# Kernel optimization log

Measured on AMD Instinct MI355X. Metric: run time of the kernel, lower is better.

The kernel has to match this reference:

```python
import jax, jax.numpy as jnp
import numpy as np

B, S, D, H, E, K, F = 8, 2048, 1024, 16, 32, 8, 1024
HD = D // H
EPS = 1e-5


def _ln(x, scale, bias):
    m = jnp.mean(x, axis=-1, keepdims=True)
    v = jnp.mean(jnp.square(x - m), axis=-1, keepdims=True)
    return (x - m) * jax.lax.rsqrt(v + EPS) * scale + bias


def setup_inputs() -> dict:
    key = jax.random.key(0)
    ks = jax.random.split(key, 14)
    w = lambda k, shp: jax.random.normal(k, shp, jnp.float32) * 0.02
    return {
        "hidden_states": jax.random.normal(ks[0], (B, S, D), jnp.float32),
        "ln1_scale": jnp.ones((D,), jnp.float32),
        "ln1_bias": jnp.zeros((D,), jnp.float32),
        "wq": w(ks[1], (D, D)), "bq": jnp.zeros((D,), jnp.float32),
        "wk": w(ks[2], (D, D)), "bk": jnp.zeros((D,), jnp.float32),
        "wv": w(ks[3], (D, D)), "bv": jnp.zeros((D,), jnp.float32),
        "ln2_scale": jnp.ones((D,), jnp.float32),
        "ln2_bias": jnp.zeros((D,), jnp.float32),
        "router_w": w(ks[4], (D, E)), "router_b": jnp.zeros((E,), jnp.float32),
        "w1": w(ks[5], (E, D, F)), "b1": jnp.zeros((E, F), jnp.float32),
        "w2": w(ks[6], (E, F, D)), "b2": jnp.zeros((E, D), jnp.float32),
    }


def reference(hidden_states, ln1_scale, ln1_bias, wq, bq, wk, bk, wv, bv,
              ln2_scale, ln2_bias, router_w, router_b, w1, b1, w2, b2):
    # --- attention sub-block (faithful to source: scores are [B,S,H,H]) ---
    x = _ln(hidden_states, ln1_scale, ln1_bias)
    q = (x @ wq + bq).reshape(B, S, H, HD)
    k = (x @ wk + bk).reshape(B, S, H, HD)
    v = (x @ wv + bv).reshape(B, S, H, HD)
    scores = jnp.einsum('bshd,bsgd->bshg', q, k) / np.sqrt(HD).astype(np.float32)
    probs = jax.nn.softmax(scores, axis=-1)
    ctx = jnp.einsum('bshg,bsgd->bshd', probs, v).reshape(B, S, D)
    h1 = hidden_states + ctx
    # --- MoE sub-block: per-token top-K of E experts ---
    x2 = _ln(h1, ln2_scale, ln2_bias)
    router_probs = jax.nn.softmax(x2 @ router_w + router_b, axis=-1)  # [B,S,E]
    top_w, top_i = jax.lax.top_k(router_probs, K)
    top_w = top_w / jnp.sum(top_w, axis=-1, keepdims=True)
    # dense per-token gate over experts (zero for unselected)
    gates = jnp.sum(jax.nn.one_hot(top_i, E, dtype=x2.dtype) * top_w[..., None], axis=-2)  # [B,S,E]
    moe = jnp.zeros_like(x2)
    for e in range(E):  # fixed small expert set; unrolled under jit
        h = jax.nn.gelu(x2 @ w1[e] + b1[e], approximate=False)
        moe = moe + gates[..., e:e + 1] * (h @ w2[e] + b2[e])
    return h1 + moe
```

## Files before the change

kernel.cpp:

```cpp
#include <hip/hip_runtime.h>
#include <hip/hip_bf16.h>
#include <stdint.h>

#define TOK 16384
#define DD  1024
#define NE  32

typedef unsigned short u16;
typedef __attribute__((ext_vector_type(8))) short short8;
typedef __attribute__((ext_vector_type(8))) unsigned short u16x8;
typedef __attribute__((ext_vector_type(4))) float f32x4;

__device__ __forceinline__ u16 f2bf(float f) {
  unsigned int u = __float_as_uint(f);
  u += 0x7fffu + ((u >> 16) & 1u);
  return (u16)(u >> 16);
}
__device__ __forceinline__ float bf2f(u16 h) {
  return __uint_as_float(((unsigned int)h) << 16);
}
__device__ __forceinline__ void gload16(const void* g, void* l) {
  __builtin_amdgcn_global_load_lds((const __attribute__((address_space(1))) void*)g,
                                   (__attribute__((address_space(3))) void*)l, 16, 0, 0);
}
__device__ __forceinline__ float fast_gelu(float v) {
  float s = v * 0.70710678118f;
  float a = fabsf(s);
  float t = 1.0f / fmaf(0.3275911f, a, 1.0f);
  float poly = t * fmaf(t, fmaf(t, fmaf(t, fmaf(t, 1.061405429f, -1.453152027f),
                                        1.421413741f), -0.284496736f), 0.254829592f);
  float er = 1.0f - poly * __expf(-s * s);
  er = copysignf(er, s);
  return 0.5f * v * (1.0f + er);
}

__global__ __launch_bounds__(256) void k_transpose(const float* __restrict__ src,
                                                   u16* __restrict__ dst, int R, int C) {
  __shared__ float tile[32][33];
  size_t mb = (size_t)blockIdx.z * R * C;
  int c0 = blockIdx.x * 32, r0 = blockIdx.y * 32;
  int tx = threadIdx.x, ty = threadIdx.y;
#pragma unroll
  for (int i = 0; i < 4; i++)
    tile[ty + i * 8][tx] = src[mb + (size_t)(r0 + ty + i * 8) * C + c0 + tx];
  __syncthreads();
#pragma unroll
  for (int i = 0; i < 4; i++) {
    float v = tile[tx][ty + i * 8];
    dst[mb + (size_t)(c0 + ty + i * 8) * R + r0 + tx] = f2bf(v);
  }
}

__global__ __launch_bounds__(256) void k_transpose_split(const float* __restrict__ src,
                                                         u16* __restrict__ hi,
                                                         u16* __restrict__ lo, int R, int C) {
  __shared__ float tile[32][33];
  int c0 = blockIdx.x * 32, r0 = blockIdx.y * 32;
  int tx = threadIdx.x, ty = threadIdx.y;
#pragma unroll
  for (int i = 0; i < 4; i++)
    tile[ty + i * 8][tx] = src[(size_t)(r0 + ty + i * 8) * C + c0 + tx];
  __syncthreads();
#pragma unroll
  for (int i = 0; i < 4; i++) {
    float v = tile[tx][ty + i * 8];
    u16 h = f2bf(v);
    u16 l = f2bf(v - bf2f(h));
    size_t idx = (size_t)(c0 + ty + i * 8) * R + r0 + tx;
    hi[idx] = h;
    lo[idx] = l;
  }
}

__global__ __launch_bounds__(256) void k_ln1(const float* __restrict__ x,
                                             const float* __restrict__ sc,
                                             const float* __restrict__ bi,
                                             u16* __restrict__ ohi, u16* __restrict__ olo) {
  __shared__ float red[10];
  int t = blockIdx.x, tid = threadIdx.x;
  size_t base = (size_t)t * DD + tid * 4;
  float4 v = *(const float4*)(x + base);
  float s1 = v.x + v.y + v.z + v.w;
  float s2 = v.x * v.x + v.y * v.y + v.z * v.z + v.w * v.w;
  for (int o = 1; o < 64; o <<= 1) { s1 += __shfl_xor(s1, o, 64); s2 += __shfl_xor(s2, o, 64); }
  int wid = tid >> 6;
  if ((tid & 63) == 0) { red[wid * 2] = s1; red[wid * 2 + 1] = s2; }
  __syncthreads();
  if (tid == 0) {
    float a = 0, b = 0;
    for (int i = 0; i < 4; i++) { a += red[i * 2]; b += red[i * 2 + 1]; }
    float mean = a * (1.f / DD);
    float var = b * (1.f / DD) - mean * mean;
    red[8] = mean; red[9] = rsqrtf(var + 1e-5f);
  }
  __syncthreads();
  float mean = red[8], rs = red[9];
  int e0 = tid * 4;
  float xv[4] = {v.x, v.y, v.z, v.w};
  ushort4 oh, ol;
  u16* ph = (u16*)&oh; u16* pl = (u16*)&ol;
#pragma unroll
  for (int i = 0; i < 4; i++) {
    float f = (xv[i] - mean) * rs * sc[e0 + i] + bi[e0 + i];
    u16 h = f2bf(f);
    ph[i] = h;
    pl[i] = f2bf(f - bf2f(h));
  }
  *(ushort4*)(ohi + base) = oh;
  *(ushort4*)(olo + base) = ol;
}

__global__ __launch_bounds__(256) void k_attn(
    const float* __restrict__ hidden, const float* __restrict__ qb,
    const float* __restrict__ kb, const float* __restrict__ vb,
    const float* __restrict__ ln2s, const float* __restrict__ ln2b,
    float* __restrict__ out, u16* __restrict__ x2hi, u16* __restrict__ x2lo) {
  __shared__ float qs[16][68], ks[16][68], vs[16][68];
  __shared__ float probs[16][17];
  __shared__ float red[12];
  int t = blockIdx.x, tid = threadIdx.x;
  size_t base = (size_t)t * DD + tid * 4;
  int hh = tid >> 4, dd = (tid & 15) * 4;
  {
    float4 q4 = *(const float4*)(qb + base);
    float4 k4 = *(const float4*)(kb + base);
    float4 v4 = *(const float4*)(vb + base);
    qs[hh][dd + 0] = q4.x; qs[hh][dd + 1] = q4.y; qs[hh][dd + 2] = q4.z; qs[hh][dd + 3] = q4.w;
    ks[hh][dd + 0] = k4.x; ks[hh][dd + 1] = k4.y; ks[hh][dd + 2] = k4.z; ks[hh][dd + 3] = k4.w;
    vs[hh][dd + 0] = v4.x; vs[hh][dd + 1] = v4.y; vs[hh][dd + 2] = v4.z; vs[hh][dd + 3] = v4.w;
  }
  __syncthreads();
  {
    int g = tid & 15;
    float s = 0.f;
#pragma unroll
    for (int d = 0; d < 64; d++) s += qs[hh][d] * ks[g][d];
    s *= 0.125f;
    float mx = s;
    for (int o = 1; o < 16; o <<= 1) mx = fmaxf(mx, __shfl_xor(mx, o, 16));
    float p = __expf(s - mx);
    float sm = p;
    for (int o = 1; o < 16; o <<= 1) sm += __shfl_xor(sm, o, 16);
    probs[hh][g] = p / sm;
  }
  __syncthreads();
  float c0 = 0, c1 = 0, c2 = 0, c3 = 0;
#pragma unroll
  for (int g = 0; g < 16; g++) {
    float pw = probs[hh][g];
    c0 += pw * vs[g][dd + 0]; c1 += pw * vs[g][dd + 1];
    c2 += pw * vs[g][dd + 2]; c3 += pw * vs[g][dd + 3];
  }
  float4 hv = *(const float4*)(hidden + base);
  float h0 = hv.x + c0, h1 = hv.y + c1, h2 = hv.z + c2, h3 = hv.w + c3;
  { float4 o4; o4.x = h0; o4.y = h1; o4.z = h2; o4.w = h3; *(float4*)(out + base) = o4; }
  float s1 = h0 + h1 + h2 + h3;
  float s2 = h0 * h0 + h1 * h1 + h2 * h2 + h3 * h3;
  for (int o = 1; o < 64; o <<= 1) { s1 += __shfl_xor(s1, o, 64); s2 += __shfl_xor(s2, o, 64); }
  int wid = tid >> 6;
  if ((tid & 63) == 0) { red[wid * 2] = s1; red[wid * 2 + 1] = s2; }
  __syncthreads();
  if (tid == 0) {
    float a = 0, b = 0;
    for (int i = 0; i < 4; i++) { a += red[i * 2]; b += red[i * 2 + 1]; }
    float mean = a * (1.f / DD);
    float var = b * (1.f / DD) - mean * mean;
    red[8] = mean; red[9] = rsqrtf(var + 1e-5f);
  }
  __syncthreads();
  float mean = red[8], rs = red[9];
  int e0 = tid * 4;
  float hvv[4] = {h0, h1, h2, h3};
  ushort4 oh, ol;
  u16* ph = (u16*)&oh; u16* pl = (u16*)&ol;
#pragma unroll
  for (int i = 0; i < 4; i++) {
    float f = (hvv[i] - mean) * rs * ln2s[e0 + i] + ln2b[e0 + i];
    u16 h = f2bf(f);
    ph[i] = h;
    pl[i] = f2bf(f - bf2f(h));
  }
  *(ushort4*)(x2hi + base) = oh;
  *(ushort4*)(x2lo + base) = ol;
}

__global__ __launch_bounds__(256) void k_router(
    const u16* __restrict__ Xhi, const u16* __restrict__ Xlo,
    const u16* __restrict__ Bh_, const u16* __restrict__ Bl_,
    const float* __restrict__ rb, float* __restrict__ logits) {
  __shared__ alignas(16) u16 Ah[64 * 32], Al[64 * 32], Bh[32 * 32], Bl[32 * 32];
  int tid = threadIdx.x;
  int w = tid >> 6, lane = tid & 63;
  int t0 = (int)blockIdx.x * 64;
  int row = tid >> 2, q = tid & 3;
  int cb = tid & 127, rowb = cb >> 2, qb2 = cb & 3;
  f32x4 acc[2];
  acc[0] = (f32x4)0.f; acc[1] = (f32x4)0.f;
  const int la = lane & 15, lk = (lane >> 4) * 8;
  const int m0 = w * 16;
  for (int kt = 0; kt < 32; kt++) {
    int k0 = kt * 32;
    __syncthreads();
    gload16(Xhi + (size_t)(t0 + row) * DD + k0 + q * 8, (char*)Ah + tid * 16);
    gload16(Xlo + (size_t)(t0 + row) * DD + k0 + q * 8, (char*)Al + tid * 16);
    if (tid < 128)
      gload16(Bh_ + (size_t)rowb * DD + k0 + qb2 * 8, (char*)Bh + cb * 16);
    else
      gload16(Bl_ + (size_t)rowb * DD + k0 + qb2 * 8, (char*)Bl + cb * 16);
    __syncthreads();
    short8 ah = *(const short8*)&Ah[(m0 + la) * 32 + lk];
    short8 al = *(const short8*)&Al[(m0 + la) * 32 + lk];
#pragma unroll
    for (int n = 0; n < 2; n++) {
      short8 bh = *(const short8*)&Bh[(n * 16 + la) * 32 + lk];
      short8 bl = *(const short8*)&Bl[(n * 16 + la) * 32 + lk];
      acc[n] = __builtin_amdgcn_mfma_f32_16x16x32_bf16(ah, bh, acc[n], 0, 0, 0);
      acc[n] = __builtin_amdgcn_mfma_f32_16x16x32_bf16(ah, bl, acc[n], 0, 0, 0);
      acc[n] = __builtin_amdgcn_mfma_f32_16x16x32_bf16(al, bh, acc[n], 0, 0, 0);
    }
  }
  int rl4 = (lane >> 4) * 4;
#pragma unroll
  for (int n = 0; n < 2; n++) {
    int col = n * 16 + la;
    float bias = rb[col];
#pragma unroll
    for (int r = 0; r < 4; r++) {
      int grow = t0 + m0 + rl4 + r;
      logits[(size_t)grow * NE + col] = acc[n][r] + bias;
    }
  }
}

__global__ void k_zero32(int* p) { int i = threadIdx.x; if (i < 32) p[i] = 0; }

__global__ __launch_bounds__(256) void k_topk(
    const float* __restrict__ logits, int* __restrict__ counts,
    int* __restrict__ lists, int* __restrict__ slots, float* __restrict__ gsel) {
  int tid = threadIdx.x;
  int t = blockIdx.x * 8 + (tid >> 5);
  int e = tid & 31;
  int sub = (tid >> 5) & 1;
  float l = logits[(size_t)t * NE + e];
  float mx = l;
  for (int o = 1; o < 32; o <<= 1) mx = fmaxf(mx, __shfl_xor(mx, o, 32));
  float p = __expf(l - mx);
  float sm = p;
  for (int o = 1; o < 32; o <<= 1) sm += __shfl_xor(sm, o, 32);
  p /= sm;
  bool sel = false;
#pragma unroll
  for (int r = 0; r < 8; r++) {
    float bv = sel ? -1.f : p;
    int bi_ = e;
    for (int o = 1; o < 32; o <<= 1) {
      float ov = __shfl_xor(bv, o, 32);
      int oi = __shfl_xor(bi_, o, 32);
      if (ov > bv || (ov == bv && oi < bi_)) { bv = ov; bi_ = oi; }
    }
    if (e == bi_) sel = true;
  }
  float ts = sel ? p : 0.f;
  for (int o = 1; o < 32; o <<= 1) ts += __shfl_xor(ts, o, 32);
  unsigned long long bm = __ballot(sel);
  unsigned m32 = (unsigned)(bm >> (sub * 32));
  if (sel) {
    int j = __popc(m32 & ((1u << e) - 1u));
    int pos = atomicAdd(&counts[e], 1);
    lists[(size_t)e * TOK + pos] = t;
    slots[t * 8 + j] = (e << 14) | pos;
    gsel[t * 8 + j] = p / ts;
  }
}

__global__ void k_scan(const int* __restrict__ counts, int* __restrict__ segoff) {
  if (threadIdx.x == 0) { int s = 0; for (int e = 0; e < NE; e++) { segoff[e] = s; s += counts[e]; } }
}

__global__ __launch_bounds__(256) void k_gemm_p(
    const u16* __restrict__ Ahi, const u16* __restrict__ Alo,
    const u16* __restrict__ qkvT,
    const float* __restrict__ bq, const float* __restrict__ bk, const float* __restrict__ bv,
    float* __restrict__ Cbase) {
  constexpr int KD = 1024;
  __shared__ alignas(16) u16 As[2][2][128 * 32];
  __shared__ alignas(16) u16 Bs[2][2][128 * 32];
  const int tid = threadIdx.x;
  const int w = tid >> 6, lane = tid & 63;
  const int bm = blockIdx.x, bn = blockIdx.y, z = blockIdx.z;
  const u16* Bhi = qkvT + (size_t)z * (2u * KD * KD);
  const u16* Blo = Bhi + (size_t)KD * KD;
  const float* bias = (z == 0) ? bq : (z == 1) ? bk : bv;
  float* C = Cbase + (size_t)z * TOK * KD;

  int rowA[2], qA[2], rowB[2];
#pragma unroll
  for (int i = 0; i < 2; i++) {
    int c = (w * 2 + i) * 64 + lane;
    int r = c >> 2;
    qA[i] = (c & 3) ^ ((c >> 3) & 3);
    rowB[i] = bn * 128 + r;
    rowA[i] = bm * 128 + r;
  }

  auto stage = [&](int buf, int k0) {
#pragma unroll
    for (int i = 0; i < 2; i++) {
      size_t ga = (size_t)rowA[i] * KD + k0 + qA[i] * 8;
      size_t gb = (size_t)rowB[i] * KD + k0 + qA[i] * 8;
      int lo_off = (w * 2 + i) * 1024;
      gload16(Ahi + ga, (char*)&As[buf][0][0] + lo_off);
      gload16(Alo + ga, (char*)&As[buf][1][0] + lo_off);
      gload16(Bhi + gb, (char*)&Bs[buf][0][0] + lo_off);
      gload16(Blo + gb, (char*)&Bs[buf][1][0] + lo_off);
    }
  };

  f32x4 acc[4][4];
#pragma unroll
  for (int m = 0; m < 4; m++)
#pragma unroll
    for (int n = 0; n < 4; n++) acc[m][n] = (f32x4)0.f;

  const int wr = (w >> 1) * 64, wc = (w & 1) * 64;
  const int la = lane & 15;
  const int sA = (((lane >> 4) ^ (((wr + la) >> 1) & 3)) * 8);
  const int sB = (((lane >> 4) ^ (((wc + la) >> 1) & 3)) * 8);

  stage(0, 0);
  __syncthreads();
  for (int kt = 0; kt < 32; kt++) {
    const int cur = kt & 1;
    if (kt + 1 < 32) stage(cur ^ 1, (kt + 1) * 32);
    short8 ah[4], al[4], bh[4], bl[4];
#pragma unroll
    for (int m = 0; m < 4; m++) {
      ah[m] = *(const short8*)&As[cur][0][(wr + m * 16 + la) * 32 + sA];
      al[m] = *(const short8*)&As[cur][1][(wr + m * 16 + la) * 32 + sA];
    }
#pragma unroll
    for (int n = 0; n < 4; n++) {
      bh[n] = *(const short8*)&Bs[cur][0][(wc + n * 16 + la) * 32 + sB];
      bl[n] = *(const short8*)&Bs[cur][1][(wc + n * 16 + la) * 32 + sB];
    }
#pragma unroll
    for (int m = 0; m < 4; m++)
#pragma unroll
      for (int n = 0; n < 4; n++) {
        acc[m][n] = __builtin_amdgcn_mfma_f32_16x16x32_bf16(ah[m], bh[n], acc[m][n], 0, 0, 0);
        acc[m][n] = __builtin_amdgcn_mfma_f32_16x16x32_bf16(ah[m], bl[n], acc[m][n], 0, 0, 0);
        acc[m][n] = __builtin_amdgcn_mfma_f32_16x16x32_bf16(al[m], bh[n], acc[m][n], 0, 0, 0);
      }
    __syncthreads();
  }

  const int rl4 = (lane >> 4) * 4;
#pragma unroll
  for (int m = 0; m < 4; m++) {
#pragma unroll
    for (int n = 0; n < 4; n++) {
      const int col = bn * 128 + wc + n * 16 + la;
      const float bvv = bias[col];
      f32x4 a4 = acc[m][n];
#pragma unroll
      for (int r = 0; r < 4; r++) {
        const int grow = bm * 128 + wr + m * 16 + rl4 + r;
        C[(size_t)grow * KD + col] = a4[r] + bvv;
      }
    }
  }
}

__global__ __launch_bounds__(256) void k_gemm1(
    const u16* __restrict__ A, const u16* __restrict__ BT, const float* __restrict__ bias,
    u16* __restrict__ Cb, const int* __restrict__ lists, const int* __restrict__ counts,
    const int* __restrict__ segoff) {
  constexpr int KD = 1024;
  __shared__ alignas(16) u16 As[2][128 * 32];
  __shared__ alignas(16) u16 Bs[2][128 * 32];

  int e = (int)blockIdx.z;
  int count = counts[e];
  if ((int)blockIdx.x * 128 >= count) return;
  const int* list = lists + (size_t)e * TOK;
  int so = segoff[e];
  const u16* Bp = BT + (size_t)e * (KD * KD);
  const float* bp = bias + (size_t)e * KD;

  const int tid = threadIdx.x;
  const int w = tid >> 6, lane = tid & 63;
  const int bm = blockIdx.x, bn = blockIdx.y;

  int rowA[2], qA[2], rowB[2];
#pragma unroll
  for (int i = 0; i < 2; i++) {
    int c = (w * 2 + i) * 64 + lane;
    int r = c >> 2;
    qA[i] = (c & 3) ^ ((c >> 3) & 3);
    rowB[i] = bn * 128 + r;
    int rr = bm * 128 + r;
    rowA[i] = (rr < count) ? list[rr] : 0;
  }

  auto stage = [&](int buf, int k0) {
#pragma unroll
    for (int i = 0; i < 2; i++) {
      gload16(A + (size_t)rowA[i] * KD + k0 + qA[i] * 8,
              (char*)&As[buf][0] + (w * 2 + i) * 1024);
      gload16(Bp + (size_t)rowB[i] * KD + k0 + qA[i] * 8,
              (char*)&Bs[buf][0] + (w * 2 + i) * 1024);
    }
  };

  f32x4 acc[4][4];
#pragma unroll
  for (int m = 0; m < 4; m++)
#pragma unroll
    for (int n = 0; n < 4; n++) acc[m][n] = (f32x4)0.f;

  const int wr = (w >> 1) * 64, wc = (w & 1) * 64;
  const int la = lane & 15;
  const int sA = (((lane >> 4) ^ (((wr + la) >> 1) & 3)) * 8);
  const int sB = (((lane >> 4) ^ (((wc + la) >> 1) & 3)) * 8);

  stage(0, 0);
  __syncthreads();
#pragma unroll 2
  for (int kt = 0; kt < 32; kt++) {
    const int cur = kt & 1;
    if (kt + 1 < 32) stage(cur ^ 1, (kt + 1) * 32);
    short8 af[4], bf8[4];
#pragma unroll
    for (int m = 0; m < 4; m++)
      af[m] = *(const short8*)&As[cur][(wr + m * 16 + la) * 32 + sA];
#pragma unroll
    for (int n = 0; n < 4; n++)
      bf8[n] = *(const short8*)&Bs[cur][(wc + n * 16 + la) * 32 + sB];
#pragma unroll
    for (int m = 0; m < 4; m++)
#pragma unroll
      for (int n = 0; n < 4; n++)
        acc[m][n] = __builtin_amdgcn_mfma_f32_16x16x32_bf16(af[m], bf8[n], acc[m][n], 0, 0, 0);
    __syncthreads();
  }

  const int rl4 = (lane >> 4) * 4;
#pragma unroll
  for (int m = 0; m < 4; m++) {
#pragma unroll
    for (int n = 0; n < 4; n++) {
      const int col = bn * 128 + wc + n * 16 + la;
      const float bvv = bp[col];
      f32x4 a4 = acc[m][n];
#pragma unroll
      for (int r = 0; r < 4; r++) {
        const int grow = bm * 128 + wr + m * 16 + rl4 + r;
        if (grow < count)
          Cb[(size_t)(so + grow) * KD + col] = f2bf(fast_gelu(a4[r] + bvv));
      }
    }
  }
}

__global__ __launch_bounds__(256) void k_gemm2(
    const u16* __restrict__ A, const u16* __restrict__ BT, const float* __restrict__ bias,
    u16* __restrict__ out2, const int* __restrict__ counts, const int* __restrict__ segoff,
    int col0, int C) {
  constexpr int KD = 1024;
  __shared__ alignas(16) u16 As[2][128 * 32];
  __shared__ alignas(16) u16 Bs[2][128 * 32];

  int e = (int)blockIdx.z;
  int count = counts[e];
  if ((int)blockIdx.x * 128 >= count) return;
  int so = segoff[e];
  const u16* Bp = BT + (size_t)e * (KD * KD);
  const float* bp = bias + (size_t)e * KD;

  const int tid = threadIdx.x;
  const int w = tid >> 6, lane = tid & 63;
  const int bm = blockIdx.x, bn = blockIdx.y;

  int rowA[2], qA[2], rowB[2];
#pragma unroll
  for (int i = 0; i < 2; i++) {
    int c = (w * 2 + i) * 64 + lane;
    int r = c >> 2;
    qA[i] = (c & 3) ^ ((c >> 3) & 3);
    rowB[i] = col0 + bn * 128 + r;
    int rr = bm * 128 + r;
    rowA[i] = so + ((rr < count) ? rr : 0);
  }

  auto stage = [&](int buf, int k0) {
#pragma unroll
    for (int i = 0; i < 2; i++) {
      gload16(A + (size_t)rowA[i] * KD + k0 + qA[i] * 8,
              (char*)&As[buf][0] + (w * 2 + i) * 1024);
      gload16(Bp + (size_t)rowB[i] * KD + k0 + qA[i] * 8,
              (char*)&Bs[buf][0] + (w * 2 + i) * 1024);
    }
  };

  f32x4 acc[4][4];
#pragma unroll
  for (int m = 0; m < 4; m++)
#pragma unroll
    for (int n = 0; n < 4; n++) acc[m][n] = (f32x4)0.f;

  const int wr = (w >> 1) * 64, wc = (w & 1) * 64;
  const int la = lane & 15;
  const int sA = (((lane >> 4) ^ (((wr + la) >> 1) & 3)) * 8);
  const int sB = (((lane >> 4) ^ (((wc + la) >> 1) & 3)) * 8);

  stage(0, 0);
  __syncthreads();
#pragma unroll 2
  for (int kt = 0; kt < 32; kt++) {
    const int cur = kt & 1;
    if (kt + 1 < 32) stage(cur ^ 1, (kt + 1) * 32);
    short8 af[4], bf8[4];
#pragma unroll
    for (int m = 0; m < 4; m++)
      af[m] = *(const short8*)&As[cur][(wr + m * 16 + la) * 32 + sA];
#pragma unroll
    for (int n = 0; n < 4; n++)
      bf8[n] = *(const short8*)&Bs[cur][(wc + n * 16 + la) * 32 + sB];
#pragma unroll
    for (int m = 0; m < 4; m++)
#pragma unroll
      for (int n = 0; n < 4; n++)
        acc[m][n] = __builtin_amdgcn_mfma_f32_16x16x32_bf16(af[m], bf8[n], acc[m][n], 0, 0, 0);
    __syncthreads();
  }

  const int rl4 = (lane >> 4) * 4;
#pragma unroll
  for (int m = 0; m < 4; m++) {
#pragma unroll
    for (int n = 0; n < 4; n++) {
      const int lcol = bn * 128 + wc + n * 16 + la;
      const float bvv = bp[col0 + lcol];
      f32x4 a4 = acc[m][n];
#pragma unroll
      for (int r = 0; r < 4; r++) {
        const int grow = bm * 128 + wr + m * 16 + rl4 + r;
        if (grow < count)
          out2[(size_t)(so + grow) * C + lcol] = f2bf(a4[r] + bvv);
      }
    }
  }
}

__global__ __launch_bounds__(256) void k_gather(
    const float* __restrict__ gsel, const int* __restrict__ slots,
    const int* __restrict__ segoff, const u16* __restrict__ out2,
    float* __restrict__ out, int col0, int C, int cshift) {
  int tid4 = threadIdx.x * 4;
  int tpb = 1024 >> cshift;
  int t = blockIdx.x * tpb + (tid4 >> cshift);
  int c4 = tid4 & (C - 1);
  float a0 = 0, a1 = 0, a2 = 0, a3 = 0;
#pragma unroll
  for (int j = 0; j < 8; j++) {
    int s = slots[t * 8 + j];
    float g = gsel[t * 8 + j];
    int seg = segoff[s >> 14] + (s & 16383);
    ushort4 v4 = *(const ushort4*)(out2 + (size_t)seg * C + c4);
    a0 += g * bf2f(v4.x); a1 += g * bf2f(v4.y);
    a2 += g * bf2f(v4.z); a3 += g * bf2f(v4.w);
  }
  size_t ob = (size_t)t * DD + col0 + c4;
  float4 o = *(const float4*)(out + ob);
  o.x += a0; o.y += a1; o.z += a2; o.w += a3;
  *(float4*)(out + ob) = o;
}

extern "C" void kernel_launch(void* const* d_in, const int* in_sizes, int n_in,
                              void* d_out, int out_size, void* d_ws, size_t ws_size,
                              hipStream_t stream) {
  (void)in_sizes; (void)n_in; (void)out_size;
  const float* hidden = (const float*)d_in[0];
  const float* ln1s = (const float*)d_in[1];
  const float* ln1b = (const float*)d_in[2];
  const float* wq = (const float*)d_in[3];
  const float* bq = (const float*)d_in[4];
  const float* wk = (const float*)d_in[5];
  const float* bk = (const float*)d_in[6];
  const float* wv = (const float*)d_in[7];
  const float* bv = (const float*)d_in[8];
  const float* ln2s = (const float*)d_in[9];
  const float* ln2b = (const float*)d_in[10];
  const float* rw = (const float*)d_in[11];
  const float* rb = (const float*)d_in[12];
  const float* w1 = (const float*)d_in[13];
  const float* b1 = (const float*)d_in[14];
  const float* w2 = (const float*)d_in[15];
  const float* b2 = (const float*)d_in[16];
  float* out = (float*)d_out;

  char* wsp = (char*)d_ws;
  size_t off = 0;
  auto alloc = [&](size_t b) -> void* {
    void* p = wsp + off;
    off += (b + 255) & ~(size_t)255;
    return p;
  };
  u16* wT = (u16*)alloc((size_t)NE * DD * DD * 2);
  int* slots = (int*)alloc((size_t)TOK * 8 * 4);
  float* gsel = (float*)alloc((size_t)TOK * 8 * 4);
  int* counts = (int*)alloc(NE * 4);
  int* segoff = (int*)alloc((NE + 1) * 4);
  u16* rwTh = (u16*)alloc((size_t)NE * DD * 2);
  u16* rwTl = (u16*)alloc((size_t)NE * DD * 2);
  char* pool = (char*)alloc((size_t)TOK * 8 * DD * 2);
  u16* qkvT = (u16*)pool;
  u16* x_lo = (u16*)(pool + 12u * 1024 * 1024);
  float* qkv = (float*)(pool + 44u * 1024 * 1024);
  float* qbuf = qkv;
  float* kbuf = qkv + (size_t)TOK * DD;
  float* vbuf = qkv + 2 * (size_t)TOK * DD;
  u16* h_buf = (u16*)pool;
  size_t tail0 = off;
  u16* x2hi = (u16*)alloc((size_t)TOK * DD * 2);
  float* logits = (float*)alloc((size_t)TOK * NE * 4);
  int* lists = (int*)alloc((size_t)NE * TOK * 4);

  const size_t ROWS = (size_t)TOK * 8;
  size_t cap = (ws_size > tail0) ? ws_size - tail0 : 0;
  int C;
  if (cap >= ROWS * 1024 * 2) C = 1024;
  else if (cap >= ROWS * 512 * 2) C = 512;
  else if (cap >= ROWS * 256 * 2) C = 256;
  else C = 128;
  u16* out2 = (u16*)(wsp + tail0);
  int cshift = 31 - __builtin_clz((unsigned)C);

  dim3 tb32(32, 8, 1);
  k_zero32<<<1, 64, 0, stream>>>(counts);
  k_transpose_split<<<dim3(32, 32, 1), tb32, 0, stream>>>(wq, qkvT, qkvT + (size_t)DD * DD, DD, DD);
  k_transpose_split<<<dim3(32, 32, 1), tb32, 0, stream>>>(wk, qkvT + 2 * (size_t)DD * DD, qkvT + 3 * (size_t)DD * DD, DD, DD);
  k_transpose_split<<<dim3(32, 32, 1), tb32, 0, stream>>>(wv, qkvT + 4 * (size_t)DD * DD, qkvT + 5 * (size_t)DD * DD, DD, DD);
  k_transpose_split<<<dim3(1, 32, 1), tb32, 0, stream>>>(rw, rwTh, rwTl, DD, NE);
  k_transpose<<<dim3(32, 32, NE), tb32, 0, stream>>>(w1, wT, DD, DD);
  k_ln1<<<TOK, 256, 0, stream>>>(hidden, ln1s, ln1b, x2hi, x_lo);
  k_gemm_p<<<dim3(128, 8, 3), 256, 0, stream>>>(x2hi, x_lo, qkvT, bq, bk, bv, qkv);
  k_attn<<<TOK, 256, 0, stream>>>(hidden, qbuf, kbuf, vbuf, ln2s, ln2b, out, x2hi, x_lo);
  k_router<<<TOK / 64, 256, 0, stream>>>(x2hi, x_lo, rwTh, rwTl, rb, logits);
  k_topk<<<TOK / 8, 256, 0, stream>>>(logits, counts, lists, slots, gsel);
  k_scan<<<1, 32, 0, stream>>>(counts, segoff);
  k_gemm1<<<dim3(128, 8, NE), 256, 0, stream>>>(x2hi, wT, b1, h_buf, lists, counts, segoff);
  k_transpose<<<dim3(32, 32, NE), tb32, 0, stream>>>(w2, wT, DD, DD);
  for (int c0 = 0; c0 < DD; c0 += C) {
    k_gemm2<<<dim3(128, C / 128, NE), 256, 0, stream>>>(h_buf, wT, b2, out2, counts, segoff, c0, C);
    k_gather<<<TOK >> (10 - cshift), 256, 0, stream>>>(gsel, slots, segoff, out2, out, c0, C, cshift);
  }
}
```

Before: 2.063 ms.

## Triple-buffer LDS staging in expert GEMMs with vmcnt-based waits

Both expert GEMM kernels move from double to triple LDS buffering with a prefetch distance of two k-tiles. Each iteration waits with explicit s_waitcnt vmcnt on only the older tile's loads and uses a single barrier instead of two __syncthreads. The aim is to hide more global-load latency and cut synchronisation per iteration. In exchange, LDS use per block grows by half, which can reduce occupancy, and correctness now rests on the hand-written vmcnt counts.

After: 2.130 ms. 3.3% more time.

```diff
diff --git a/kernel.cpp b/kernel.cpp
--- a/kernel.cpp
+++ b/kernel.cpp
@@ -8,7 +8,6 @@
 
 typedef unsigned short u16;
 typedef __attribute__((ext_vector_type(8))) short short8;
-typedef __attribute__((ext_vector_type(8))) unsigned short u16x8;
 typedef __attribute__((ext_vector_type(4))) float f32x4;
 
 __device__ __forceinline__ u16 f2bf(float f) {
@@ -376,8 +375,8 @@
     u16* __restrict__ Cb, const int* __restrict__ lists, const int* __restrict__ counts,
     const int* __restrict__ segoff) {
   constexpr int KD = 1024;
-  __shared__ alignas(16) u16 As[2][128 * 32];
-  __shared__ alignas(16) u16 Bs[2][128 * 32];
+  __shared__ alignas(16) u16 As[3][128 * 32];
+  __shared__ alignas(16) u16 Bs[3][128 * 32];
 
   int e = (int)blockIdx.z;
   int count = counts[e];
@@ -424,24 +423,29 @@
   const int sB = (((lane >> 4) ^ (((wc + la) >> 1) & 3)) * 8);
 
   stage(0, 0);
-  __syncthreads();
-#pragma unroll 2
+  stage(1, 32);
+  int cur = 0;
   for (int kt = 0; kt < 32; kt++) {
-    const int cur = kt & 1;
-    if (kt + 1 < 32) stage(cur ^ 1, (kt + 1) * 32);
+    if (kt < 31) asm volatile("s_waitcnt vmcnt(4)" ::: "memory");
+    else         asm volatile("s_waitcnt vmcnt(0)" ::: "memory");
+    __builtin_amdgcn_s_barrier();
+    asm volatile("" ::: "memory");
+    if (kt + 2 < 32) stage((kt + 2) % 3, (kt + 2) * 32);
+    const u16* Ab = &As[cur][0];
+    const u16* Bb = &Bs[cur][0];
     short8 af[4], bf8[4];
 #pragma unroll
     for (int m = 0; m < 4; m++)
-      af[m] = *(const short8*)&As[cur][(wr + m * 16 + la) * 32 + sA];
+      af[m] = *(const short8*)&Ab[(wr + m * 16 + la) * 32 + sA];
 #pragma unroll
     for (int n = 0; n < 4; n++)
-      bf8[n] = *(const short8*)&Bs[cur][(wc + n * 16 + la) * 32 + sB];
+      bf8[n] = *(const short8*)&Bb[(wc + n * 16 + la) * 32 + sB];
 #pragma unroll
     for (int m = 0; m < 4; m++)
 #pragma unroll
       for (int n = 0; n < 4; n++)
         acc[m][n] = __builtin_amdgcn_mfma_f32_16x16x32_bf16(af[m], bf8[n], acc[m][n], 0, 0, 0);
-    __syncthreads();
+    cur = (cur == 2) ? 0 : cur + 1;
   }
 
   const int rl4 = (lane >> 4) * 4;
@@ -467,8 +471,8 @@
     u16* __restrict__ out2, const int* __restrict__ counts, const int* __restrict__ segoff,
     int col0, int C) {
   constexpr int KD = 1024;
-  __shared__ alignas(16) u16 As[2][128 * 32];
-  __shared__ alignas(16) u16 Bs[2][128 * 32];
+  __shared__ alignas(16) u16 As[3][128 * 32];
+  __shared__ alignas(16) u16 Bs[3][128 * 32];
 
   int e = (int)blockIdx.z;
   int count = counts[e];
@@ -514,24 +518,29 @@
   const int sB = (((lane >> 4) ^ (((wc + la) >> 1) & 3)) * 8);
 
   stage(0, 0);
-  __syncthreads();
-#pragma unroll 2
+  stage(1, 32);
+  int cur = 0;
   for (int kt = 0; kt < 32; kt++) {
-    const int cur = kt & 1;
-    if (kt + 1 < 32) stage(cur ^ 1, (kt + 1) * 32);
+    if (kt < 31) asm volatile("s_waitcnt vmcnt(4)" ::: "memory");
+    else         asm volatile("s_waitcnt vmcnt(0)" ::: "memory");
+    __builtin_amdgcn_s_barrier();
+    asm volatile("" ::: "memory");
+    if (kt + 2 < 32) stage((kt + 2) % 3, (kt + 2) * 32);
+    const u16* Ab = &As[cur][0];
+    const u16* Bb = &Bs[cur][0];
     short8 af[4], bf8[4];
 #pragma unroll
     for (int m = 0; m < 4; m++)
-      af[m] = *(const short8*)&As[cur][(wr + m * 16 + la) * 32 + sA];
+      af[m] = *(const short8*)&Ab[(wr + m * 16 + la) * 32 + sA];
 #pragma unroll
     for (int n = 0; n < 4; n++)
-      bf8[n] = *(const short8*)&Bs[cur][(wc + n * 16 + la) * 32 + sB];
+      bf8[n] = *(const short8*)&Bb[(wc + n * 16 + la) * 32 + sB];
 #pragma unroll
     for (int m = 0; m < 4; m++)
 #pragma unroll
       for (int n = 0; n < 4; n++)
         acc[m][n] = __builtin_amdgcn_mfma_f32_16x16x32_bf16(af[m], bf8[n], acc[m][n], 0, 0, 0);
-    __syncthreads();
+    cur = (cur == 2) ? 0 : cur + 1;
   }
 
   const int rl4 = (lane >> 4) * 4;
```
